# Performance work log

Hardware: AMD Instinct MI355X
Metric: run time of the kernel (lower is better)

Reference implementation:

```python
import jax, jax.numpy as jnp
import numpy as np

N = 100000      # nodes (== hyperedges, H is square: adjacency-derived incidence)
NNZ = 3200000   # nonzeros in H
IN, HID, OUT = 512, 16, 64


def setup_inputs() -> dict:
    key = jax.random.key(0)
    ks = jax.random.split(key, 8)
    row = jax.random.randint(ks[0], (NNZ,), 0, N)
    col = jax.random.randint(ks[1], (NNZ,), 0, N)
    values = jnp.ones((NNZ,), dtype=jnp.float32)
    X = jax.random.normal(ks[2], (N, IN), dtype=jnp.float32)
    W1 = jax.random.normal(ks[3], (HID, IN), dtype=jnp.float32) * 0.05
    b1 = jax.random.normal(ks[4], (HID,), dtype=jnp.float32) * 0.05
    W2 = jax.random.normal(ks[5], (OUT, HID), dtype=jnp.float32) * 0.05
    b2 = jax.random.normal(ks[6], (OUT,), dtype=jnp.float32) * 0.05
    return {"row": row, "col": col, "values": values, "X": X,
            "W1": W1, "b1": b1, "W2": W2, "b2": b2}


def reference(row, col, values, X, W1, b1, W2, b2):
    # Degrees: d_V = H.sum(1) over rows, d_E = H.sum(0) over cols
    d_V = jax.ops.segment_sum(values, row, num_segments=N)
    d_E = jax.ops.segment_sum(values, col, num_segments=N)
    dv = d_V ** -0.5          # D_V^-1/2 diagonal
    de = d_E ** -1.0          # D_E^-1 diagonal (W = I, folded in)

    def conv(Y):
        # D_V^-1/2 @ H @ D_E^-1 @ H^T @ D_V^-1/2 @ Y, via edge-list SpMMs
        Y1 = Y * dv[:, None]
        # Z = H^T @ Y1 : scatter v * Y1[row] into hyperedge bins (col)
        Z = jax.ops.segment_sum(values[:, None] * Y1[row], col, num_segments=N)
        Z = Z * de[:, None]
        # O = H @ Z : scatter v * Z[col] back into node bins (row)
        O = jax.ops.segment_sum(values[:, None] * Z[col], row, num_segments=N)
        return O * dv[:, None]

    # dropout is identity in eval mode
    H1 = jax.nn.relu(conv(X @ W1.T + b1))      # [N, HID]
    out = conv(H1 @ W2.T + b2)                  # [N, OUT]
    return out
```

## Files before the change

kernel.cpp:

```cpp
#include <hip/hip_runtime.h>

#define NN 100000
#define NNZ 3200000
#define DIN 512
#define DHID 16
#define DOUT 64
#define NBUK 391
#define BCAP 9216
#define EPB 4096
#define NBLK_A ((NNZ + EPB - 1) / EPB)

#define GLOBAL_AS __attribute__((address_space(1)))
#define LDS_AS    __attribute__((address_space(3)))


__global__ __launch_bounds__(256) void init_cur_kernel(
    int* __restrict__ cur_c, int* __restrict__ cur_r) {
    int i = blockIdx.x * 256 + threadIdx.x;
    if (i < NBUK) { cur_c[i] = i * BCAP; cur_r[i] = i * BCAP; }
}

__global__ __launch_bounds__(256) void bucket_scatter_kernel(
    const int* __restrict__ row, const int* __restrict__ col,
    int* __restrict__ cur_c, int* __restrict__ cur_r,
    int* __restrict__ stgc, int* __restrict__ stgr) {
    __shared__ int stage[EPB];
    __shared__ unsigned short binOf[EPB];
    __shared__ int hist[512], scn[256], lof[512], curb[512], gdelta[512];
    int side = blockIdx.y;
    const int* key = side ? row : col;
    const int* oth = side ? col : row;
    int* gcur = side ? cur_r : cur_c;
    int* gstg = side ? stgr : stgc;
    int tid = threadIdx.x;
    int m = NNZ - blockIdx.x * EPB; if (m > EPB) m = EPB;
    int e0 = blockIdx.x * EPB + tid;

    hist[tid] = 0; hist[tid + 256] = 0;
    __syncthreads();
    #pragma unroll 4
    for (int u = 0; u < EPB / 256; ++u) {
        if (tid + u * 256 < m) atomicAdd(&hist[key[e0 + u * 256] >> 8], 1);
    }
    __syncthreads();
    int s0 = hist[2 * tid], s1 = hist[2 * tid + 1];
    int ps = s0 + s1;
    scn[tid] = ps;
    __syncthreads();
    for (int d = 1; d < 256; d <<= 1) {
        int t = (tid >= d) ? scn[tid - d] : 0;
        __syncthreads();
        scn[tid] += t;
        __syncthreads();
    }
    int excl = scn[tid] - ps;
    lof[2 * tid] = excl;
    lof[2 * tid + 1] = excl + s0;
    curb[2 * tid] = excl;
    curb[2 * tid + 1] = excl + s0;
    if (2 * tid < NBUK)
        gdelta[2 * tid] = (s0 ? atomicAdd(&gcur[2 * tid], s0) : (2 * tid) * BCAP) - excl;
    if (2 * tid + 1 < NBUK)
        gdelta[2 * tid + 1] = (s1 ? atomicAdd(&gcur[2 * tid + 1], s1) : (2 * tid + 1) * BCAP) - (excl + s0);
    __syncthreads();
    #pragma unroll 2
    for (int u = 0; u < EPB / 256; ++u) {
        if (tid + u * 256 < m) {
            int e = e0 + u * 256;
            int k = key[e], o2 = oth[e];
            int bin = k >> 8;
            int pos = atomicAdd(&curb[bin], 1);
            stage[pos] = ((k & 255) << 17) | o2;
            binOf[pos] = (unsigned short)bin;
        }
    }
    __syncthreads();
    for (int i = tid; i < m; i += 256) {
        int bin = binOf[i];
        int dst = gdelta[bin] + i;
        if (dst < (bin + 1) * BCAP) gstg[dst] = stage[i];
    }
}

__global__ __launch_bounds__(256) void bucket_finalize_kernel(
    const int* __restrict__ cur_c, const int* __restrict__ cur_r,
    const int* __restrict__ stgc, const int* __restrict__ stgr,
    int* __restrict__ adjc, int* __restrict__ adjr,
    int* __restrict__ os_c, int* __restrict__ oe_c,
    int* __restrict__ os_r, int* __restrict__ oe_r,
    float* __restrict__ dee, float* __restrict__ dvv) {
    int side = blockIdx.y;
    const int* curv = side ? cur_r : cur_c;
    const int* stg = side ? stgr : stgc;
    int* adj = side ? adjr : adjc;
    int* os = side ? os_r : os_c;
    int* oe = side ? oe_r : oe_c;
    __shared__ int E[BCAP];
    __shared__ int hist[256], cur[256], scn[256];
    int b = blockIdx.x, tid = threadIdx.x;
    int base = b * BCAP;
    int m = curv[b] - base;
    if (m > BCAP) m = BCAP;
    hist[tid] = 0;
    __syncthreads();
    for (int i = tid; i < m; i += 256) {
        int ev = stg[base + i];
        E[i] = ev;
        atomicAdd(&hist[ev >> 17], 1);
    }
    __syncthreads();
    int x = hist[tid];
    scn[tid] = x;
    __syncthreads();
    for (int d = 1; d < 256; d <<= 1) {
        int t = (tid >= d) ? scn[tid - d] : 0;
        __syncthreads();
        scn[tid] += t;
        __syncthreads();
    }
    int excl = scn[tid] - x;
    cur[tid] = excl;
    __syncthreads();
    for (int i = tid; i < m; i += 256) {
        int ev = E[i];
        int nl = ev >> 17;
        int pos = atomicAdd(&cur[nl], 1);
        adj[base + pos] = ev & 0x1FFFF;
    }
    int n = (b << 8) + tid;
    if (n < NN) {
        os[n] = base + excl;
        oe[n] = base + excl + x;
        float xf = (float)x;
        if (side == 0) dee[n] = x > 0 ? 1.0f / xf : 0.f;
        else           dvv[n] = x > 0 ? rsqrtf(xf) : 0.f;
    }
}

__global__ __launch_bounds__(256) void gemm1_kernel(
    const float* __restrict__ X, const float* __restrict__ W1,
    const float* __restrict__ b1, const float* __restrict__ dvv,
    float* __restrict__ Yv) {
    __shared__ float W1s[16 * 516];
    __shared__ float Xs[16 * 260];
    int tid = threadIdx.x;
    for (int it = 0; it < 8; ++it) {
        int idx = (it * 256 + tid) << 2;
        int h = idx >> 9, k = idx & 511;
        __builtin_amdgcn_global_load_lds(
            (const GLOBAL_AS void*)(W1 + idx),
            (LDS_AS void*)(W1s + h * 516 + k), 16, 0, 0);
    }
    int n0 = blockIdx.x << 4;
    int n = tid >> 4, h = tid & 15;
    float4 a4 = make_float4(0.f, 0.f, 0.f, 0.f);
    for (int ck = 0; ck < 512; ck += 256) {
        __syncthreads();
        for (int it = 0; it < 4; ++it) {
            int idx = (it * 256 + tid) << 2;
            int r = idx >> 8, k = idx & 255;
            __builtin_amdgcn_global_load_lds(
                (const GLOBAL_AS void*)(X + (size_t)(n0 + r) * DIN + ck + k),
                (LDS_AS void*)(Xs + r * 260 + k), 16, 0, 0);
        }
        __syncthreads();
        const float4* xr = reinterpret_cast<const float4*>(Xs + n * 260);
        const float4* wr = reinterpret_cast<const float4*>(W1s + h * 516 + ck);
        #pragma unroll 8
        for (int k4 = 0; k4 < 64; ++k4) {
            float4 xv = xr[k4], wv = wr[k4];
            a4.x = fmaf(xv.x, wv.x, a4.x);
            a4.y = fmaf(xv.y, wv.y, a4.y);
            a4.z = fmaf(xv.z, wv.z, a4.z);
            a4.w = fmaf(xv.w, wv.w, a4.w);
        }
    }
    float acc = (a4.x + a4.y) + (a4.z + a4.w);
    int node = n0 + n;
    Yv[node * DHID + h] = (acc + b1[h]) * dvv[node];
}

template<int MODE, int FUSE1, int FUSEOUT>
__global__ __launch_bounds__(256) void gather16_kernel(
    const int* __restrict__ os, const int* __restrict__ oe,
    const int* __restrict__ adj, const float* __restrict__ src,
    const float* __restrict__ sc, const float* __restrict__ src1,
    const float* __restrict__ sc1, float* __restrict__ dst,
    float* __restrict__ dst1, const float* __restrict__ W2,
    const float* __restrict__ b2, const float* __restrict__ g1,
    float* __restrict__ outp) {
    __shared__ float W2t[16 * 64];
    __shared__ float b2s[64];
    int tid = threadIdx.x;
    if (FUSEOUT) {
        #pragma unroll
        for (int q = 0; q < 4; ++q) {
            int idx = (tid << 2) + q;
            int o = idx >> 4, h = idx & 15;
            W2t[h * 64 + o] = W2[idx];
        }
        if (tid < 64) b2s[tid] = b2[tid];
        __syncthreads();
    }
    int t = blockIdx.x * 256 + tid;
    int n = t >> 4, sub = (t >> 3) & 1, f2 = t & 7;
    const float2* src2 = reinterpret_cast<const float2*>(src);
    float2 a0 = make_float2(0.f, 0.f);
    float2 a1 = make_float2(0.f, 0.f);
    float2 a2 = make_float2(0.f, 0.f);
    float2 a3 = make_float2(0.f, 0.f);
    float acc1 = 0.f;
    int pe = oe[n];
    int p = os[n] + sub;
    for (; p + 6 < pe; p += 8) {
        int j0 = adj[p], j1 = adj[p + 2], j2 = adj[p + 4], j3 = adj[p + 6];
        float2 s0 = src2[(j0 << 3) | f2];
        float2 s1 = src2[(j1 << 3) | f2];
        float2 s2 = src2[(j2 << 3) | f2];
        float2 s3 = src2[(j3 << 3) | f2];
        a0.x += s0.x; a0.y += s0.y;
        a1.x += s1.x; a1.y += s1.y;
        a2.x += s2.x; a2.y += s2.y;
        a3.x += s3.x; a3.y += s3.y;
        if (FUSE1 && f2 == 0) acc1 += (src1[j0] + src1[j1]) + (src1[j2] + src1[j3]);
    }
    for (; p < pe; p += 2) {
        int j0 = adj[p];
        float2 s0 = src2[(j0 << 3) | f2];
        a0.x += s0.x; a0.y += s0.y;
        if (FUSE1 && f2 == 0) acc1 += src1[j0];
    }
    float2 acc = make_float2((a0.x + a1.x) + (a2.x + a3.x),
                             (a0.y + a1.y) + (a2.y + a3.y));
    acc.x += __shfl_xor(acc.x, 8);
    acc.y += __shfl_xor(acc.y, 8);
    if (FUSE1 && f2 == 0) acc1 += __shfl_xor(acc1, 8);
    if (FUSEOUT) {
        float s = sc[n];
        float T[16];
        #pragma unroll
        for (int q = 0; q < 8; ++q) {
            T[2 * q]     = s * __shfl(acc.x, q, 16);
            T[2 * q + 1] = s * __shfl(acc.y, q, 16);
        }
        int l = tid & 15;
        float gn = g1[n];
        float4 o4 = make_float4(0.f, 0.f, 0.f, 0.f);
        #pragma unroll
        for (int h = 0; h < DHID; ++h) {
            float4 w = *reinterpret_cast<const float4*>(&W2t[h * 64 + 4 * l]);
            o4.x = fmaf(T[h], w.x, o4.x);
            o4.y = fmaf(T[h], w.y, o4.y);
            o4.z = fmaf(T[h], w.z, o4.z);
            o4.w = fmaf(T[h], w.w, o4.w);
        }
        float4 bb = *reinterpret_cast<const float4*>(&b2s[4 * l]);
        o4.x = fmaf(gn, bb.x, o4.x);
        o4.y = fmaf(gn, bb.y, o4.y);
        o4.z = fmaf(gn, bb.z, o4.z);
        o4.w = fmaf(gn, bb.w, o4.w);
        reinterpret_cast<float4*>(outp)[(n << 4) | l] = o4;
    } else if (sub == 0) {
        float s = sc[n];
        if (MODE == 1) {
            acc.x *= s; acc.y *= s;
        } else {
            acc.x = s * fmaxf(s * acc.x, 0.f);
            acc.y = s * fmaxf(s * acc.y, 0.f);
        }
        reinterpret_cast<float2*>(dst)[(n << 3) | f2] = acc;
        if (FUSE1 && f2 == 0) dst1[n] = acc1 * sc1[n];
    }
}

extern "C" void kernel_launch(void* const* d_in, const int* in_sizes, int n_in,
                              void* d_out, int out_size, void* d_ws, size_t ws_size,
                              hipStream_t stream) {
    const int*   row    = (const int*)d_in[0];
    const int*   col    = (const int*)d_in[1];
    const float* X      = (const float*)d_in[3];
    const float* W1     = (const float*)d_in[4];
    const float* b1     = (const float*)d_in[5];
    const float* W2     = (const float*)d_in[6];
    const float* b2     = (const float*)d_in[7];
    float* out = (float*)d_out;

    char* ws = (char*)d_ws;
    size_t o = 0;
    auto alloc = [&](size_t elems) {
        void* p = ws + o; o += (elems * 4 + 15) & ~size_t(15); return p;
    };

    int*   cur_c = (int*)alloc(NBUK);
    int*   cur_r = (int*)alloc(NBUK);
    int*   os_c  = (int*)alloc(NN);
    int*   oe_c  = (int*)alloc(NN);
    int*   os_r  = (int*)alloc(NN);
    int*   oe_r  = (int*)alloc(NN);
    float* dvv   = (float*)alloc(NN);
    float* dee   = (float*)alloc(NN);
    float* ue    = (float*)alloc(NN);
    float* gv    = (float*)alloc(NN);
    int*   stgc  = (int*)alloc((size_t)NBUK * BCAP);
    int*   stgr  = (int*)alloc((size_t)NBUK * BCAP);
    int*   adjc  = (int*)alloc((size_t)NBUK * BCAP);
    int*   adjr  = (int*)alloc((size_t)NBUK * BCAP);
    float* Yv    = (float*)alloc((size_t)NN * DHID);
    float* Z1    = (float*)alloc((size_t)NN * DHID);
    float* Sv    = (float*)alloc((size_t)NN * DHID);
    float* Z2    = (float*)alloc((size_t)NN * DHID);

    init_cur_kernel<<<dim3((NBUK + 255) / 256), dim3(256), 0, stream>>>(cur_c, cur_r);
    bucket_scatter_kernel<<<dim3(NBLK_A, 2), dim3(256), 0, stream>>>(
        row, col, cur_c, cur_r, stgc, stgr);
    bucket_finalize_kernel<<<dim3(NBUK, 2), dim3(256), 0, stream>>>(
        cur_c, cur_r, stgc, stgr, adjc, adjr, os_c, oe_c, os_r, oe_r, dee, dvv);

    gemm1_kernel<<<dim3(NN / 16), dim3(256), 0, stream>>>(X, W1, b1, dvv, Yv);

    int gblk = NN * 16 / 256;
    gather16_kernel<1, 1, 0><<<dim3(gblk), dim3(256), 0, stream>>>(
        os_c, oe_c, adjc, Yv, dee, dvv, dee, Z1, ue,
        nullptr, nullptr, nullptr, nullptr);
    gather16_kernel<2, 1, 0><<<dim3(gblk), dim3(256), 0, stream>>>(
        os_r, oe_r, adjr, Z1, dvv, ue, dvv, Sv, gv,
        nullptr, nullptr, nullptr, nullptr);

    gather16_kernel<1, 0, 0><<<dim3(gblk), dim3(256), 0, stream>>>(
        os_c, oe_c, adjc, Sv, dee, nullptr, nullptr, Z2, nullptr,
        nullptr, nullptr, nullptr, nullptr);
    gather16_kernel<1, 0, 1><<<dim3(gblk), dim3(256), 0, stream>>>(
        os_r, oe_r, adjr, Z2, dvv, nullptr, nullptr, nullptr, nullptr,
        W2, b2, gv, out);
}
```

Before: 361.1 us.

## Use float4 gathers with 4-way edge split and double-buffer X tiles in gemm1

The 16-wide gather kernel now has each node's 16 lanes split 4 ways over the edge list, each lane loading a float4 (4 lanes cover a 16-float row), instead of 2 ways with float2 loads. The result needs two xor-shuffle reduction steps instead of one. This raises memory-level parallelism and widens each load, at the cost of more shuffles and more lanes sitting idle on short adjacency lists. Separately, gemm1 issues both halves of the X tile into two LDS buffers up front so the second load overlaps the first half's compute, using more LDS per block.

```diff
diff --git a/kernel.cpp b/kernel.cpp
--- a/kernel.cpp
+++ b/kernel.cpp
@@ -142,7 +142,8 @@
     const float* __restrict__ b1, const float* __restrict__ dvv,
     float* __restrict__ Yv) {
     __shared__ float W1s[16 * 516];
-    __shared__ float Xs[16 * 260];
+    __shared__ float Xs0[16 * 260];
+    __shared__ float Xs1[16 * 260];
     int tid = threadIdx.x;
     for (int it = 0; it < 8; ++it) {
         int idx = (it * 256 + tid) << 2;
@@ -152,20 +153,39 @@
             (LDS_AS void*)(W1s + h * 516 + k), 16, 0, 0);
     }
     int n0 = blockIdx.x << 4;
+    for (int it = 0; it < 4; ++it) {
+        int idx = (it * 256 + tid) << 2;
+        int r = idx >> 8, k = idx & 255;
+        __builtin_amdgcn_global_load_lds(
+            (const GLOBAL_AS void*)(X + (size_t)(n0 + r) * DIN + k),
+            (LDS_AS void*)(Xs0 + r * 260 + k), 16, 0, 0);
+    }
+    __syncthreads();
+    for (int it = 0; it < 4; ++it) {
+        int idx = (it * 256 + tid) << 2;
+        int r = idx >> 8, k = idx & 255;
+        __builtin_amdgcn_global_load_lds(
+            (const GLOBAL_AS void*)(X + (size_t)(n0 + r) * DIN + 256 + k),
+            (LDS_AS void*)(Xs1 + r * 260 + k), 16, 0, 0);
+    }
     int n = tid >> 4, h = tid & 15;
     float4 a4 = make_float4(0.f, 0.f, 0.f, 0.f);
-    for (int ck = 0; ck < 512; ck += 256) {
-        __syncthreads();
-        for (int it = 0; it < 4; ++it) {
-            int idx = (it * 256 + tid) << 2;
-            int r = idx >> 8, k = idx & 255;
-            __builtin_amdgcn_global_load_lds(
-                (const GLOBAL_AS void*)(X + (size_t)(n0 + r) * DIN + ck + k),
-                (LDS_AS void*)(Xs + r * 260 + k), 16, 0, 0);
-        }
-        __syncthreads();
-        const float4* xr = reinterpret_cast<const float4*>(Xs + n * 260);
-        const float4* wr = reinterpret_cast<const float4*>(W1s + h * 516 + ck);
+    {
+        const float4* xr = reinterpret_cast<const float4*>(Xs0 + n * 260);
+        const float4* wr = reinterpret_cast<const float4*>(W1s + h * 516);
+        #pragma unroll 8
+        for (int k4 = 0; k4 < 64; ++k4) {
+            float4 xv = xr[k4], wv = wr[k4];
+            a4.x = fmaf(xv.x, wv.x, a4.x);
+            a4.y = fmaf(xv.y, wv.y, a4.y);
+            a4.z = fmaf(xv.z, wv.z, a4.z);
+            a4.w = fmaf(xv.w, wv.w, a4.w);
+        }
+    }
+    __syncthreads();
+    {
+        const float4* xr = reinterpret_cast<const float4*>(Xs1 + n * 260);
+        const float4* wr = reinterpret_cast<const float4*>(W1s + h * 516 + 256);
         #pragma unroll 8
         for (int k4 = 0; k4 < 64; ++k4) {
             float4 xv = xr[k4], wv = wr[k4];
@@ -203,45 +223,55 @@
         __syncthreads();
     }
     int t = blockIdx.x * 256 + tid;
-    int n = t >> 4, sub = (t >> 3) & 1, f2 = t & 7;
-    const float2* src2 = reinterpret_cast<const float2*>(src);
-    float2 a0 = make_float2(0.f, 0.f);
-    float2 a1 = make_float2(0.f, 0.f);
-    float2 a2 = make_float2(0.f, 0.f);
-    float2 a3 = make_float2(0.f, 0.f);
+    int n = t >> 4, sub = (t >> 2) & 3, f4 = t & 3;
+    const float4* src4 = reinterpret_cast<const float4*>(src);
+    float4 a0 = make_float4(0.f, 0.f, 0.f, 0.f);
+    float4 a1 = make_float4(0.f, 0.f, 0.f, 0.f);
+    float4 a2 = make_float4(0.f, 0.f, 0.f, 0.f);
+    float4 a3 = make_float4(0.f, 0.f, 0.f, 0.f);
     float acc1 = 0.f;
     int pe = oe[n];
     int p = os[n] + sub;
-    for (; p + 6 < pe; p += 8) {
-        int j0 = adj[p], j1 = adj[p + 2], j2 = adj[p + 4], j3 = adj[p + 6];
-        float2 s0 = src2[(j0 << 3) | f2];
-        float2 s1 = src2[(j1 << 3) | f2];
-        float2 s2 = src2[(j2 << 3) | f2];
-        float2 s3 = src2[(j3 << 3) | f2];
-        a0.x += s0.x; a0.y += s0.y;
-        a1.x += s1.x; a1.y += s1.y;
-        a2.x += s2.x; a2.y += s2.y;
-        a3.x += s3.x; a3.y += s3.y;
-        if (FUSE1 && f2 == 0) acc1 += (src1[j0] + src1[j1]) + (src1[j2] + src1[j3]);
-    }
-    for (; p < pe; p += 2) {
+    for (; p + 12 < pe; p += 16) {
+        int j0 = adj[p], j1 = adj[p + 4], j2 = adj[p + 8], j3 = adj[p + 12];
+        float4 s0 = src4[(j0 << 2) | f4];
+        float4 s1 = src4[(j1 << 2) | f4];
+        float4 s2 = src4[(j2 << 2) | f4];
+        float4 s3 = src4[(j3 << 2) | f4];
+        a0.x += s0.x; a0.y += s0.y; a0.z += s0.z; a0.w += s0.w;
+        a1.x += s1.x; a1.y += s1.y; a1.z += s1.z; a1.w += s1.w;
+        a2.x += s2.x; a2.y += s2.y; a2.z += s2.z; a2.w += s2.w;
+        a3.x += s3.x; a3.y += s3.y; a3.z += s3.z; a3.w += s3.w;
+        if (FUSE1 && f4 == 0) acc1 += (src1[j0] + src1[j1]) + (src1[j2] + src1[j3]);
+    }
+    for (; p < pe; p += 4) {
         int j0 = adj[p];
-        float2 s0 = src2[(j0 << 3) | f2];
-        a0.x += s0.x; a0.y += s0.y;
-        if (FUSE1 && f2 == 0) acc1 += src1[j0];
-    }
-    float2 acc = make_float2((a0.x + a1.x) + (a2.x + a3.x),
-                             (a0.y + a1.y) + (a2.y + a3.y));
-    acc.x += __shfl_xor(acc.x, 8);
-    acc.y += __shfl_xor(acc.y, 8);
-    if (FUSE1 && f2 == 0) acc1 += __shfl_xor(acc1, 8);
+        float4 s0 = src4[(j0 << 2) | f4];
+        a0.x += s0.x; a0.y += s0.y; a0.z += s0.z; a0.w += s0.w;
+        if (FUSE1 && f4 == 0) acc1 += src1[j0];
+    }
+    float4 acc;
+    acc.x = (a0.x + a1.x) + (a2.x + a3.x);
+    acc.y = (a0.y + a1.y) + (a2.y + a3.y);
+    acc.z = (a0.z + a1.z) + (a2.z + a3.z);
+    acc.w = (a0.w + a1.w) + (a2.w + a3.w);
+    acc.x += __shfl_xor(acc.x, 4); acc.y += __shfl_xor(acc.y, 4);
+    acc.z += __shfl_xor(acc.z, 4); acc.w += __shfl_xor(acc.w, 4);
+    acc.x += __shfl_xor(acc.x, 8); acc.y += __shfl_xor(acc.y, 8);
+    acc.z += __shfl_xor(acc.z, 8); acc.w += __shfl_xor(acc.w, 8);
+    if (FUSE1 && f4 == 0) {
+        acc1 += __shfl_xor(acc1, 4);
+        acc1 += __shfl_xor(acc1, 8);
+    }
     if (FUSEOUT) {
         float s = sc[n];
         float T[16];
         #pragma unroll
-        for (int q = 0; q < 8; ++q) {
-            T[2 * q]     = s * __shfl(acc.x, q, 16);
-            T[2 * q + 1] = s * __shfl(acc.y, q, 16);
+        for (int q = 0; q < 4; ++q) {
+            T[4 * q + 0] = s * __shfl(acc.x, q, 16);
+            T[4 * q + 1] = s * __shfl(acc.y, q, 16);
+            T[4 * q + 2] = s * __shfl(acc.z, q, 16);
+            T[4 * q + 3] = s * __shfl(acc.w, q, 16);
         }
         int l = tid & 15;
         float gn = g1[n];
@@ -263,13 +293,15 @@
     } else if (sub == 0) {
         float s = sc[n];
         if (MODE == 1) {
-            acc.x *= s; acc.y *= s;
+            acc.x *= s; acc.y *= s; acc.z *= s; acc.w *= s;
         } else {
             acc.x = s * fmaxf(s * acc.x, 0.f);
             acc.y = s * fmaxf(s * acc.y, 0.f);
-        }
-        reinterpret_cast<float2*>(dst)[(n << 3) | f2] = acc;
-        if (FUSE1 && f2 == 0) dst1[n] = acc1 * sc1[n];
+            acc.z = s * fmaxf(s * acc.z, 0.f);
+            acc.w = s * fmaxf(s * acc.w, 0.f);
+        }
+        reinterpret_cast<float4*>(dst)[(n << 2) | f4] = acc;
+        if (FUSE1 && f4 == 0) dst1[n] = acc1 * sc1[n];
     }
 }
 
```

Measured after the change: 363.5 us. About the same (+0.6%).
